# Performance work log

Measured on AMD Instinct MI355X. Metric: run time of the kernel, lower is better.

Reference implementation:

```python
import jax, jax.numpy as jnp
import numpy as np
import math

B, S, HID = 1, 2048, 1024
H = 16
D = HID // H          # head_dim = 64
M = 128               # RFF num_features
SIGMA = 1.0
ALPHA = 0.9
NORMALIZE = True


def setup_inputs() -> dict:
    key = jax.random.key(0)
    ks = jax.random.split(key, 12)
    s = 1.0 / math.sqrt(HID)  # nn.Linear default-ish init scale
    inp = {
        "hidden_states": jax.random.normal(ks[0], (B, S, HID), dtype=jnp.float32),
        "attention_mask": jnp.zeros((B, 1, 1, S), dtype=jnp.float32),  # 0 = attend
        "Wq": jax.random.uniform(ks[1], (HID, HID), minval=-s, maxval=s, dtype=jnp.float32),
        "bq": jnp.zeros((HID,), dtype=jnp.float32),
        "Wk": jax.random.uniform(ks[2], (HID, HID), minval=-s, maxval=s, dtype=jnp.float32),
        "bk": jnp.zeros((HID,), dtype=jnp.float32),
        "Wv": jax.random.uniform(ks[3], (HID, HID), minval=-s, maxval=s, dtype=jnp.float32),
        "bv": jnp.zeros((HID,), dtype=jnp.float32),
        "Wo": jax.random.uniform(ks[4], (HID, HID), minval=-s, maxval=s, dtype=jnp.float32),
        "bo": jnp.zeros((HID,), dtype=jnp.float32),
        # RFF kernel params per head: omega ~ N(0, 1/sigma^2), phase b ~ U[0, 2pi]
        "omega": jax.random.normal(ks[5], (H, D, M), dtype=jnp.float32) / SIGMA,
        "rff_b": jax.random.uniform(ks[6], (H, M), minval=0.0, maxval=2.0 * math.pi, dtype=jnp.float32),
    }
    return inp


def _heads(x):
    # (B, S, HID) -> (B, H, S, D)
    return x.reshape(B, S, H, D).transpose(0, 2, 1, 3)


def _phi(x, omega, rff_b):
    # x: (B, H, S, D) -> (B, H, S, M) random Fourier features
    proj = jnp.einsum("bhsd,hdm->bhsm", x, omega) + rff_b[None, :, None, :]
    phi = math.sqrt(2.0 / M) * jnp.cos(proj)
    if NORMALIZE:
        phi = phi / (jnp.linalg.norm(phi, axis=-1, keepdims=True) + 1e-6)
    return phi


def reference(hidden_states, attention_mask, Wq, bq, Wk, bk, Wv, bv, Wo, bo, omega, rff_b):
    q = _heads(hidden_states @ Wq.T + bq)   # (B,H,S,D)
    k = _heads(hidden_states @ Wk.T + bk)
    v = _heads(hidden_states @ Wv.T + bv)

    qn = q / (jnp.linalg.norm(q, axis=-1, keepdims=True) + 1e-6)
    kn = k / (jnp.linalg.norm(k, axis=-1, keepdims=True) + 1e-6)

    dot_scores = jnp.einsum("bhqd,bhkd->bhqk", q, k)             # standard QK^T
    kernel_scores = jnp.einsum("bhqm,bhkm->bhqk",
                               _phi(qn, omega, rff_b),
                               _phi(kn, omega, rff_b))            # phi(Q)phi(K)^T

    scores = (ALPHA * dot_scores + (1.0 - ALPHA) * kernel_scores) / math.sqrt(D)
    scores = scores + attention_mask * -10000.0
    weights = jax.nn.softmax(scores, axis=-1)                     # dropout: eval mode (identity)

    context = jnp.einsum("bhqk,bhkd->bhqd", weights, v)
    context = context.transpose(0, 2, 1, 3).reshape(B, S, HID)
    return context @ Wo.T + bo
```

## Files before the change

kernel.cpp:

```cpp
#include <hip/hip_runtime.h>
#include <math.h>

#define S_LEN 2048
#define HID   1024
#define NH    16
#define HD    64
#define NM    128
#define CAUG  192
#define KSPL  4

constexpr float ALPHA = 0.9f;

typedef __attribute__((ext_vector_type(8))) short bf16x8;
typedef __attribute__((ext_vector_type(4))) short bf16x4;
typedef __attribute__((ext_vector_type(4))) float f32x4;
typedef __attribute__((ext_vector_type(4))) int   int4v;

#define MFMA(a,b,c) __builtin_amdgcn_mfma_f32_16x16x32_bf16(a,b,c,0,0,0)

static __device__ inline short f2bf(float f) {
    unsigned u = __float_as_uint(f);
    u += 0x7fffu + ((u >> 16) & 1u);
    return (short)(u >> 16);
}
static __device__ inline float bf2f(short s) {
    return __uint_as_float(((unsigned)(unsigned short)s) << 16);
}

__global__ __launch_bounds__(256)
void conv_kernel(const float* __restrict__ hs,
                 const float* __restrict__ Wq, const float* __restrict__ Wk,
                 const float* __restrict__ Wv, const float* __restrict__ Wo,
                 const float* __restrict__ omega,
                 short* __restrict__ hsb, short* __restrict__ wqb, short* __restrict__ wkb,
                 short* __restrict__ wvb, short* __restrict__ wob, short* __restrict__ omtb)
{
    int i = blockIdx.x * 256 + threadIdx.x;
    if (i >= 1605632) return;
    if (i >= 1572864) {
        int j = (i - 1572864) * 4;
        int h = j >> 13, rem = j & 8191;
        int d = rem >> 7, m = rem & 127;
        float4 v = *(const float4*)(omega + j);
        short* dst = omtb + ((h * 128 + m) << 6) + d;
        dst[0]       = f2bf(v.x);
        dst[64]      = f2bf(v.y);
        dst[128]     = f2bf(v.z);
        dst[192]     = f2bf(v.w);
        return;
    }
    const float* src; short* dst; int off;
    if (i < 524288) { src = hs; dst = hsb; off = i; }
    else {
        int j = i - 524288;
        int r = j >> 18;
        off = j & 262143;
        src = (r == 0) ? Wq : (r == 1) ? Wk : (r == 2) ? Wv : Wo;
        dst = (r == 0) ? wqb : (r == 1) ? wkb : (r == 2) ? wvb : wob;
    }
    float4 v = ((const float4*)src)[off];
    bf16x4 o; o[0] = f2bf(v.x); o[1] = f2bf(v.y); o[2] = f2bf(v.z); o[3] = f2bf(v.w);
    ((bf16x4*)dst)[off] = o;
}

__global__ __launch_bounds__(256)
void gemm_mfma(const short* __restrict__ A,
               const short* __restrict__ W0, const float* __restrict__ b0, void* C0,
               const short* __restrict__ W1, const float* __restrict__ b1, void* C1,
               const short* __restrict__ W2, const float* __restrict__ b2, void* C2,
               int m0_, int m1_, int m2_, int Mrows)
{
    const short* W; const float* bias; void* C; int mode;
    if (blockIdx.z == 0)      { W = W0; bias = b0; C = C0; mode = m0_; }
    else if (blockIdx.z == 1) { W = W1; bias = b1; C = C1; mode = m1_; }
    else                      { W = W2; bias = b2; C = C2; mode = m2_; }

    __shared__ short As[64][40];
    __shared__ short Bs[128][40];

    const int tid = threadIdx.x;
    const int wave = tid >> 6, lane = tid & 63;
    const int l15 = lane & 15, l4 = lane >> 4;
    const int wm = wave >> 1, wn = wave & 1;
    const int m0 = blockIdx.y * 64, n0 = blockIdx.x * 128;

    const int srow = tid >> 2;
    const int scol = (tid & 3) * 16;

    f32x4 acc[2][4];
#pragma unroll
    for (int i = 0; i < 2; ++i)
#pragma unroll
        for (int j = 0; j < 4; ++j) acc[i][j] = (f32x4){0.f,0.f,0.f,0.f};

    int4v apre, bpre0, bpre1;
    apre  = *(const int4v*)((const char*)A + (size_t)(m0 + srow) * 2048 + scol);
    bpre0 = *(const int4v*)((const char*)W + (size_t)(n0 + srow) * 2048 + scol);
    bpre1 = *(const int4v*)((const char*)W + (size_t)(n0 + 64 + srow) * 2048 + scol);

    for (int ks = 0; ks < 32; ++ks) {
        __syncthreads();
        *(int4v*)((char*)&As[0][0] + srow * 80 + scol) = apre;
        *(int4v*)((char*)&Bs[0][0] + srow * 80 + scol) = bpre0;
        *(int4v*)((char*)&Bs[0][0] + (64 + srow) * 80 + scol) = bpre1;
        __syncthreads();
        if (ks + 1 < 32) {
            const int kb = (ks + 1) * 64;
            apre  = *(const int4v*)((const char*)A + (size_t)(m0 + srow) * 2048 + kb + scol);
            bpre0 = *(const int4v*)((const char*)W + (size_t)(n0 + srow) * 2048 + kb + scol);
            bpre1 = *(const int4v*)((const char*)W + (size_t)(n0 + 64 + srow) * 2048 + kb + scol);
        }
        bf16x8 af[2], bf[4];
#pragma unroll
        for (int mi = 0; mi < 2; ++mi)
            af[mi] = *(const bf16x8*)((const char*)&As[0][0] + (wm*32 + mi*16 + l15) * 80 + l4*16);
#pragma unroll
        for (int nj = 0; nj < 4; ++nj)
            bf[nj] = *(const bf16x8*)((const char*)&Bs[0][0] + (wn*64 + nj*16 + l15) * 80 + l4*16);
#pragma unroll
        for (int mi = 0; mi < 2; ++mi)
#pragma unroll
            for (int nj = 0; nj < 4; ++nj)
                acc[mi][nj] = MFMA(af[mi], bf[nj], acc[mi][nj]);
    }

#pragma unroll
    for (int nj = 0; nj < 4; ++nj) {
        const int nglob = n0 + wn*64 + nj*16 + l15;
        const float bn = bias[nglob];
#pragma unroll
        for (int mi = 0; mi < 2; ++mi) {
            const int mbase = m0 + wm*32 + mi*16 + l4*4;
            if (mode == 0) {
#pragma unroll
                for (int r = 0; r < 4; ++r)
                    ((short*)C)[(size_t)(mbase + r) * 1024 + nglob] = f2bf(acc[mi][nj][r] + bn);
            } else if (mode == 1) {
                bf16x4 pk;
#pragma unroll
                for (int r = 0; r < 4; ++r) pk[r] = f2bf(acc[mi][nj][r] + bn);
                *(bf16x4*)((short*)C + (size_t)nglob * Mrows + mbase) = pk;
            } else {
#pragma unroll
                for (int r = 0; r < 4; ++r)
                    ((float*)C)[(size_t)(mbase + r) * 1024 + nglob] = acc[mi][nj][r] + bn;
            }
        }
    }
}

__global__ __launch_bounds__(256)
void phi2_kernel(const short* __restrict__ qbuf, const short* __restrict__ kbuf,
                 const short* __restrict__ omtb, const float* __restrict__ rffb,
                 short* __restrict__ Qa, short* __restrict__ Ka)
{
    __shared__ short om[128][72];
    __shared__ float bsh[128];

    const int src = blockIdx.z, h = blockIdx.y;
    const int s0 = blockIdx.x * 64;
    const short* X = src ? kbuf : qbuf;
    short* Out     = src ? Ka : Qa;
    const float fq   = src ? 1.0f : (ALPHA * 0.125f);
    const float fphi = src ? 1.0f : ((1.0f - ALPHA) * 0.125f);

    const int tid = threadIdx.x, wave = tid >> 6, lane = tid & 63;
    const int l15 = lane & 15, l4 = lane >> 4;

    {
        const char* gsrc = (const char*)(omtb + ((size_t)h << 13));
#pragma unroll
        for (int it = 0; it < 4; ++it) {
            int f = tid * 16 + it * 4096;
            int row = f >> 7, colb = f & 127;
            *(int4v*)((char*)&om[0][0] + row * 144 + colb) = *(const int4v*)(gsrc + f);
        }
        if (tid < 128) bsh[tid] = rffb[h * 128 + tid];
    }
    __syncthreads();

    const int srow = s0 + wave * 16 + l15;

    bf16x8 xf[2];
#pragma unroll
    for (int cs = 0; cs < 2; ++cs)
        xf[cs] = *(const bf16x8*)(X + (size_t)srow * HID + h * HD + cs * 32 + l4 * 8);

    float ss = 0.f;
#pragma unroll
    for (int cs = 0; cs < 2; ++cs)
#pragma unroll
        for (int j = 0; j < 8; ++j) { float v = bf2f(xf[cs][j]); ss = fmaf(v, v, ss); }
    ss += __shfl_xor(ss, 16);
    ss += __shfl_xor(ss, 32);
    const float inv = 1.0f / (sqrtf(ss) + 1e-6f);

    bf16x8 qn[2];
#pragma unroll
    for (int cs = 0; cs < 2; ++cs) {
        bf16x8 o, w;
#pragma unroll
        for (int j = 0; j < 8; ++j) {
            float v = bf2f(xf[cs][j]);
            o[j] = f2bf(v * inv);
            w[j] = f2bf(v * fq);
        }
        qn[cs] = o;
        *(bf16x8*)(Out + ((size_t)h * S_LEN + srow) * CAUG + cs * 32 + l4 * 8) = w;
    }

    f32x4 pacc[8];
#pragma unroll
    for (int t = 0; t < 8; ++t) pacc[t] = (f32x4){0.f,0.f,0.f,0.f};
#pragma unroll
    for (int t = 0; t < 8; ++t)
#pragma unroll
        for (int cs = 0; cs < 2; ++cs) {
            bf16x8 bf = *(const bf16x8*)((const char*)&om[0][0] + (t*16 + l15) * 144 + cs*64 + l4*16);
            pacc[t] = MFMA(qn[cs], bf, pacc[t]);
        }

    float ph[8][4];
    float ps[4] = {0.f, 0.f, 0.f, 0.f};
#pragma unroll
    for (int t = 0; t < 8; ++t) {
        const float bv = bsh[t * 16 + l15];
#pragma unroll
        for (int r = 0; r < 4; ++r) {
            float p = pacc[t][r] + bv;
            float c = 0.125f * __cosf(p);
            ph[t][r] = c;
            ps[r] = fmaf(c, c, ps[r]);
        }
    }
#pragma unroll
    for (int r = 0; r < 4; ++r) {
        ps[r] += __shfl_xor(ps[r], 1);
        ps[r] += __shfl_xor(ps[r], 2);
        ps[r] += __shfl_xor(ps[r], 4);
        ps[r] += __shfl_xor(ps[r], 8);
    }
    float inv2[4];
#pragma unroll
    for (int r = 0; r < 4; ++r) inv2[r] = fphi / (sqrtf(ps[r]) + 1e-6f);

#pragma unroll
    for (int t = 0; t < 8; ++t)
#pragma unroll
        for (int r = 0; r < 4; ++r)
            Out[((size_t)h * S_LEN + s0 + wave * 16 + l4 * 4 + r) * CAUG + 64 + t * 16 + l15]
                = f2bf(ph[t][r] * inv2[r]);
}

__global__ __launch_bounds__(128, 4)
void flash_mfma(const short* __restrict__ Qa, const short* __restrict__ Ka,
                const short* __restrict__ vt, const float* __restrict__ mask,
                short* __restrict__ Opart, float* __restrict__ Lpart)
{
    __shared__ char smem[20480];

    const int tid = threadIdx.x;
    const int wave = tid >> 6, lane = tid & 63;
    const int l15 = lane & 15, l4 = lane >> 4;
    const int h = blockIdx.y, ksp = blockIdx.z;
    const int q0 = blockIdx.x * 64 + wave * 32;

    char* Kbuf = smem;
    char* Vbuf = smem + 12288;
    char* Pb   = smem + 16384 + wave * 2048;

    bf16x8 qf[2][6];
#pragma unroll
    for (int qj = 0; qj < 2; ++qj)
#pragma unroll
        for (int cs = 0; cs < 6; ++cs)
            qf[qj][cs] = *(const bf16x8*)(Qa + ((size_t)h * 2048 + q0 + qj*16 + l15) * CAUG + cs*32 + l4*8);

    f32x4 oacc[4][2];
#pragma unroll
    for (int di = 0; di < 4; ++di)
#pragma unroll
        for (int qj = 0; qj < 2; ++qj) oacc[di][qj] = (f32x4){0.f,0.f,0.f,0.f};
    float lsum[2] = {0.f, 0.f};

    int gK[6], wrK[6];
#pragma unroll
    for (int it = 0; it < 6; ++it) {
        int f = tid * 16 + it * 2048;
        int row = f / 384, col = f - row * 384;
        gK[it] = f;
        wrK[it] = row * 384 + (col ^ ((row & 7) << 4));
    }
    int gVrow[2], gVcol[2], wrV[2];
#pragma unroll
    for (int it = 0; it < 2; ++it) {
        int f = tid * 16 + it * 2048;
        int row = f >> 6, col = f & 63;
        gVrow[it] = row; gVcol[it] = col;
        wrV[it] = row * 64 + (col ^ ((row & 3) << 4));
    }

    const char* Kg = (const char*)(Ka + (size_t)h * 2048 * CAUG);
    const char* Vg = (const char*)(vt + (size_t)h * 64 * 2048);
    const int base = ksp * 16;
    const int swP = (l15 & 3) << 4;
    const int swK = (l15 & 7) << 4;

    for (int i = 0; i < 16; ++i) {
        const int kt = base + i;
        int4v kv[6], vv[2];
        const char* kb = Kg + (size_t)kt * 12288;
#pragma unroll
        for (int it = 0; it < 6; ++it)
            kv[it] = *(const int4v*)(kb + gK[it]);
#pragma unroll
        for (int it = 0; it < 2; ++it)
            vv[it] = *(const int4v*)(Vg + (size_t)gVrow[it] * 4096 + kt * 64 + gVcol[it]);
        __syncthreads();
#pragma unroll
        for (int it = 0; it < 6; ++it) *(int4v*)(Kbuf + wrK[it]) = kv[it];
#pragma unroll
        for (int it = 0; it < 2; ++it) *(int4v*)(Vbuf + wrV[it]) = vv[it];
        __syncthreads();

        f32x4 sacc[2][2];
#pragma unroll
        for (int fi = 0; fi < 2; ++fi)
#pragma unroll
            for (int qj = 0; qj < 2; ++qj) sacc[fi][qj] = (f32x4){0.f,0.f,0.f,0.f};
#pragma unroll
        for (int cs = 0; cs < 6; ++cs) {
            bf16x8 ka[2];
#pragma unroll
            for (int fi = 0; fi < 2; ++fi)
                ka[fi] = *(const bf16x8*)(Kbuf + (fi*16 + l15)*384 + ((cs*64 + l4*16) ^ swK));
#pragma unroll
            for (int fi = 0; fi < 2; ++fi)
#pragma unroll
                for (int qj = 0; qj < 2; ++qj)
                    sacc[fi][qj] = MFMA(ka[fi], qf[qj][cs], sacc[fi][qj]);
        }
#pragma unroll
        for (int fi = 0; fi < 2; ++fi) {
            float4 mk = *(const float4*)&mask[kt*32 + fi*16 + l4*4];
            float mv[4] = {mk.x * -10000.f, mk.y * -10000.f, mk.z * -10000.f, mk.w * -10000.f};
#pragma unroll
            for (int qj = 0; qj < 2; ++qj) {
                bf16x4 pk;
#pragma unroll
                for (int r = 0; r < 4; ++r) {
                    float p = __expf(sacc[fi][qj][r] + mv[r]);
                    lsum[qj] += p;
                    pk[r] = f2bf(p);
                }
                *(bf16x4*)(Pb + (qj*16 + l15)*64 + ((fi*32 + l4*8) ^ swP)) = pk;
            }
        }
        {
            bf16x8 pb[2];
#pragma unroll
            for (int qj = 0; qj < 2; ++qj)
                pb[qj] = *(const bf16x8*)(Pb + (qj*16 + l15)*64 + ((l4*16) ^ swP));
#pragma unroll
            for (int di = 0; di < 4; ++di) {
                const int vrow = di*16 + l15;
                bf16x8 va = *(const bf16x8*)(Vbuf + vrow*64 + ((l4*16) ^ ((vrow & 3) << 4)));
#pragma unroll
                for (int qj = 0; qj < 2; ++qj)
                    oacc[di][qj] = MFMA(va, pb[qj], oacc[di][qj]);
            }
        }
    }

#pragma unroll
    for (int qj = 0; qj < 2; ++qj) {
        lsum[qj] += __shfl_xor(lsum[qj], 16);
        lsum[qj] += __shfl_xor(lsum[qj], 32);
    }

    const size_t obase = (size_t)(ksp * NH + h) * 2048 + q0;
#pragma unroll
    for (int qj = 0; qj < 2; ++qj) {
        const size_t orow = obase + qj*16 + l15;
#pragma unroll
        for (int di = 0; di < 4; ++di) {
            bf16x4 ob;
#pragma unroll
            for (int r = 0; r < 4; ++r) ob[r] = f2bf(oacc[di][qj][r]);
            *(bf16x4*)(Opart + orow * 64 + di*16 + l4*4) = ob;
        }
        if (l4 == 0) Lpart[orow] = lsum[qj];
    }
}

__global__ __launch_bounds__(256)
void merge_kernel(const short* __restrict__ Opart, const float* __restrict__ Lpart,
                  short* __restrict__ ctxb)
{
    int tt = blockIdx.x * 256 + threadIdx.x;
    int e = tt * 4;
    int d = e & 63;
    int q = (e >> 6) & 2047;
    int h = e >> 17;
    float acc[4] = {0.f, 0.f, 0.f, 0.f};
    float L = 0.f;
#pragma unroll
    for (int s = 0; s < KSPL; ++s) {
        size_t idx = (size_t)(s * NH + h) * 2048 + q;
        bf16x4 a = *(const bf16x4*)(Opart + idx * 64 + d);
        L += Lpart[idx];
#pragma unroll
        for (int r = 0; r < 4; ++r) acc[r] += bf2f(a[r]);
    }
    float inv = 1.0f / L;
    bf16x4 o;
#pragma unroll
    for (int r = 0; r < 4; ++r) o[r] = f2bf(acc[r] * inv);
    *(bf16x4*)(ctxb + (size_t)q * 1024 + h * 64 + d) = o;
}

extern "C" void kernel_launch(void* const* d_in, const int* in_sizes, int n_in,
                              void* d_out, int out_size, void* d_ws, size_t ws_size,
                              hipStream_t stream)
{
    const float* hs    = (const float*)d_in[0];
    const float* mask  = (const float*)d_in[1];
    const float* Wq    = (const float*)d_in[2];
    const float* bq    = (const float*)d_in[3];
    const float* Wk    = (const float*)d_in[4];
    const float* bk    = (const float*)d_in[5];
    const float* Wv    = (const float*)d_in[6];
    const float* bv    = (const float*)d_in[7];
    const float* Wo    = (const float*)d_in[8];
    const float* bo    = (const float*)d_in[9];
    const float* omega = (const float*)d_in[10];
    const float* rffb  = (const float*)d_in[11];
    float* out = (float*)d_out;

    short* wsS  = (short*)d_ws;
    short* hsb  = wsS;
    short* wqb  = hsb + 2097152;
    short* wkb  = wqb + 1048576;
    short* wvb  = wkb + 1048576;
    short* wob  = wvb + 1048576;
    short* qb   = wob + 1048576;
    short* kb   = qb  + 2097152;
    short* vtb  = kb  + 2097152;
    short* ctxb = vtb + 2097152;
    short* QaB  = ctxb+ 2097152;
    short* KaB  = QaB + 6291456;
    short* omtb = KaB + 6291456;
    short* OpS  = omtb+ 131072;
    float* LpF  = (float*)(OpS + 8388608);

    conv_kernel<<<6272, 256, 0, stream>>>(hs, Wq, Wk, Wv, Wo, omega,
                                          hsb, wqb, wkb, wvb, wob, omtb);
    gemm_mfma<<<dim3(8, 32, 3), 256, 0, stream>>>(hsb, wqb, bq, qb, wkb, bk, kb, wvb, bv, vtb,
                                                  0, 0, 1, S_LEN);
    phi2_kernel<<<dim3(32, 16, 2), 256, 0, stream>>>(qb, kb, omtb, rffb, QaB, KaB);
    flash_mfma<<<dim3(32, 16, KSPL), 128, 0, stream>>>(QaB, KaB, vtb, mask, OpS, LpF);
    merge_kernel<<<2048, 256, 0, stream>>>(OpS, LpF, ctxb);
    gemm_mfma<<<dim3(8, 32, 1), 256, 0, stream>>>(ctxb, wob, bo, out, wob, bo, out, wob, bo, out,
                                                  2, 2, 2, S_LEN);
}
```

Measured before the change: 135.8 us.

## Switch flash attention kernel to 32x32x16 MFMA with in-register P via permlane swap

Rewrites the attention inner loop to use 32x32x16 bf16 MFMA tiles, one per wave covering 32 queries. The softmax probabilities are packed with v_cvt_pk_bf16_f32 and rearranged with v_permlane32_swap, so the P tile no longer goes through shared memory. K and V LDS layouts change to match: K is stored unswizzled and V uses a padded 80-byte row stride, and LDS use shrinks. This aims to cut LDS traffic and MFMA instruction count, at the cost of more registers (launch bounds lowered to 3 blocks per SM) and possible LDS bank conflicts from dropping the swizzle.

```diff
diff --git a/kernel.cpp b/kernel.cpp
--- a/kernel.cpp
+++ b/kernel.cpp
@@ -11,12 +11,14 @@
 
 constexpr float ALPHA = 0.9f;
 
-typedef __attribute__((ext_vector_type(8))) short bf16x8;
-typedef __attribute__((ext_vector_type(4))) short bf16x4;
-typedef __attribute__((ext_vector_type(4))) float f32x4;
-typedef __attribute__((ext_vector_type(4))) int   int4v;
-
-#define MFMA(a,b,c) __builtin_amdgcn_mfma_f32_16x16x32_bf16(a,b,c,0,0,0)
+typedef __attribute__((ext_vector_type(8)))  short bf16x8;
+typedef __attribute__((ext_vector_type(4)))  short bf16x4;
+typedef __attribute__((ext_vector_type(4)))  float f32x4;
+typedef __attribute__((ext_vector_type(16))) float f32x16;
+typedef __attribute__((ext_vector_type(4)))  int   int4v;
+
+#define MFMA(a,b,c)   __builtin_amdgcn_mfma_f32_16x16x32_bf16(a,b,c,0,0,0)
+#define MFMA32(a,b,c) __builtin_amdgcn_mfma_f32_32x32x16_bf16(a,b,c,0,0,0)
 
 static __device__ inline short f2bf(float f) {
     unsigned u = __float_as_uint(f);
@@ -25,6 +27,12 @@
 }
 static __device__ inline float bf2f(short s) {
     return __uint_as_float(((unsigned)(unsigned short)s) << 16);
+}
+static __device__ inline f32x16 zero16() {
+    f32x16 z;
+#pragma unroll
+    for (int j = 0; j < 16; ++j) z[j] = 0.f;
+    return z;
 }
 
 __global__ __launch_bounds__(256)
@@ -252,145 +260,122 @@
                 = f2bf(ph[t][r] * inv2[r]);
 }
 
-__global__ __launch_bounds__(128, 4)
+__global__ __launch_bounds__(128, 3)
 void flash_mfma(const short* __restrict__ Qa, const short* __restrict__ Ka,
                 const short* __restrict__ vt, const float* __restrict__ mask,
                 short* __restrict__ Opart, float* __restrict__ Lpart)
 {
-    __shared__ char smem[20480];
+    __shared__ char smem[17408];
+    char* Kbuf = smem;
+    char* Vbuf = smem + 12288;
 
     const int tid = threadIdx.x;
     const int wave = tid >> 6, lane = tid & 63;
-    const int l15 = lane & 15, l4 = lane >> 4;
-    const int h = blockIdx.y, ksp = blockIdx.z;
+    const int l31 = lane & 31, h = lane >> 5;
+    const int hd = blockIdx.y, ksp = blockIdx.z;
     const int q0 = blockIdx.x * 64 + wave * 32;
 
-    char* Kbuf = smem;
-    char* Vbuf = smem + 12288;
-    char* Pb   = smem + 16384 + wave * 2048;
-
-    bf16x8 qf[2][6];
-#pragma unroll
-    for (int qj = 0; qj < 2; ++qj)
-#pragma unroll
-        for (int cs = 0; cs < 6; ++cs)
-            qf[qj][cs] = *(const bf16x8*)(Qa + ((size_t)h * 2048 + q0 + qj*16 + l15) * CAUG + cs*32 + l4*8);
-
-    f32x4 oacc[4][2];
-#pragma unroll
-    for (int di = 0; di < 4; ++di)
-#pragma unroll
-        for (int qj = 0; qj < 2; ++qj) oacc[di][qj] = (f32x4){0.f,0.f,0.f,0.f};
-    float lsum[2] = {0.f, 0.f};
-
-    int gK[6], wrK[6];
+    bf16x8 qf[12];
+    {
+        const char* qrow = (const char*)Qa + ((size_t)hd * 2048 + q0 + l31) * 384 + h * 16;
+#pragma unroll
+        for (int cs = 0; cs < 12; ++cs)
+            qf[cs] = *(const bf16x8*)(qrow + cs * 32);
+    }
+
+    f32x16 oacc0 = zero16(), oacc1 = zero16();
+    float lsum = 0.f;
+
+    int gK[6];
 #pragma unroll
     for (int it = 0; it < 6; ++it) {
-        int f = tid * 16 + it * 2048;
-        int row = f / 384, col = f - row * 384;
-        gK[it] = f;
-        wrK[it] = row * 384 + (col ^ ((row & 7) << 4));
-    }
-    int gVrow[2], gVcol[2], wrV[2];
-#pragma unroll
-    for (int it = 0; it < 2; ++it) {
-        int f = tid * 16 + it * 2048;
-        int row = f >> 6, col = f & 63;
-        gVrow[it] = row; gVcol[it] = col;
-        wrV[it] = row * 64 + (col ^ ((row & 3) << 4));
-    }
-
-    const char* Kg = (const char*)(Ka + (size_t)h * 2048 * CAUG);
-    const char* Vg = (const char*)(vt + (size_t)h * 64 * 2048);
+        int L = (it * 128 + tid) * 16;
+        int cs = L >> 10, rem = L & 1023;
+        gK[it] = (rem >> 5) * 384 + cs * 32 + (rem & 16);
+    }
+    int gVrow[3], vcolA[3], wV[3];
+#pragma unroll
+    for (int it = 0; it < 3; ++it) {
+        int p = (it * 128 + tid) * 16;
+        int vr = p / 80, vc = p - vr * 80;
+        gVrow[it] = vr; vcolA[it] = vc; wV[it] = vr * 80 + vc;
+    }
+    const bool v2ok = (tid < 64);
+
+    const char* Kg = (const char*)Ka + (size_t)hd * 2048 * 384;
+    const char* Vg = (const char*)vt + (size_t)hd * 64 * 4096;
     const int base = ksp * 16;
-    const int swP = (l15 & 3) << 4;
-    const int swK = (l15 & 7) << 4;
 
     for (int i = 0; i < 16; ++i) {
         const int kt = base + i;
-        int4v kv[6], vv[2];
-        const char* kb = Kg + (size_t)kt * 12288;
+        int4v kv[6];
+        {
+            const char* kb = Kg + (size_t)kt * 12288;
+#pragma unroll
+            for (int it = 0; it < 6; ++it) kv[it] = *(const int4v*)(kb + gK[it]);
+        }
+        int4v vv0 = *(const int4v*)(Vg + (size_t)gVrow[0] * 4096 + kt * 64 + vcolA[0]);
+        int4v vv1 = *(const int4v*)(Vg + (size_t)gVrow[1] * 4096 + kt * 64 + vcolA[1]);
+        int4v vv2;
+        if (v2ok) vv2 = *(const int4v*)(Vg + (size_t)gVrow[2] * 4096 + kt * 64 + vcolA[2]);
+        __syncthreads();
 #pragma unroll
         for (int it = 0; it < 6; ++it)
-            kv[it] = *(const int4v*)(kb + gK[it]);
-#pragma unroll
-        for (int it = 0; it < 2; ++it)
-            vv[it] = *(const int4v*)(Vg + (size_t)gVrow[it] * 4096 + kt * 64 + gVcol[it]);
+            *(int4v*)(Kbuf + (it * 128 + tid) * 16) = kv[it];
+        *(int4v*)(Vbuf + wV[0]) = vv0;
+        *(int4v*)(Vbuf + wV[1]) = vv1;
+        if (v2ok) *(int4v*)(Vbuf + wV[2]) = vv2;
         __syncthreads();
-#pragma unroll
-        for (int it = 0; it < 6; ++it) *(int4v*)(Kbuf + wrK[it]) = kv[it];
-#pragma unroll
-        for (int it = 0; it < 2; ++it) *(int4v*)(Vbuf + wrV[it]) = vv[it];
-        __syncthreads();
-
-        f32x4 sacc[2][2];
-#pragma unroll
-        for (int fi = 0; fi < 2; ++fi)
-#pragma unroll
-            for (int qj = 0; qj < 2; ++qj) sacc[fi][qj] = (f32x4){0.f,0.f,0.f,0.f};
-#pragma unroll
-        for (int cs = 0; cs < 6; ++cs) {
-            bf16x8 ka[2];
-#pragma unroll
-            for (int fi = 0; fi < 2; ++fi)
-                ka[fi] = *(const bf16x8*)(Kbuf + (fi*16 + l15)*384 + ((cs*64 + l4*16) ^ swK));
-#pragma unroll
-            for (int fi = 0; fi < 2; ++fi)
-#pragma unroll
-                for (int qj = 0; qj < 2; ++qj)
-                    sacc[fi][qj] = MFMA(ka[fi], qf[qj][cs], sacc[fi][qj]);
-        }
-#pragma unroll
-        for (int fi = 0; fi < 2; ++fi) {
-            float4 mk = *(const float4*)&mask[kt*32 + fi*16 + l4*4];
-            float mv[4] = {mk.x * -10000.f, mk.y * -10000.f, mk.z * -10000.f, mk.w * -10000.f};
-#pragma unroll
-            for (int qj = 0; qj < 2; ++qj) {
-                bf16x4 pk;
-#pragma unroll
-                for (int r = 0; r < 4; ++r) {
-                    float p = __expf(sacc[fi][qj][r] + mv[r]);
-                    lsum[qj] += p;
-                    pk[r] = f2bf(p);
-                }
-                *(bf16x4*)(Pb + (qj*16 + l15)*64 + ((fi*32 + l4*8) ^ swP)) = pk;
-            }
-        }
-        {
-            bf16x8 pb[2];
-#pragma unroll
-            for (int qj = 0; qj < 2; ++qj)
-                pb[qj] = *(const bf16x8*)(Pb + (qj*16 + l15)*64 + ((l4*16) ^ swP));
-#pragma unroll
-            for (int di = 0; di < 4; ++di) {
-                const int vrow = di*16 + l15;
-                bf16x8 va = *(const bf16x8*)(Vbuf + vrow*64 + ((l4*16) ^ ((vrow & 3) << 4)));
-#pragma unroll
-                for (int qj = 0; qj < 2; ++qj)
-                    oacc[di][qj] = MFMA(va, pb[qj], oacc[di][qj]);
-            }
-        }
-    }
-
-#pragma unroll
-    for (int qj = 0; qj < 2; ++qj) {
-        lsum[qj] += __shfl_xor(lsum[qj], 16);
-        lsum[qj] += __shfl_xor(lsum[qj], 32);
-    }
-
-    const size_t obase = (size_t)(ksp * NH + h) * 2048 + q0;
-#pragma unroll
-    for (int qj = 0; qj < 2; ++qj) {
-        const size_t orow = obase + qj*16 + l15;
-#pragma unroll
-        for (int di = 0; di < 4; ++di) {
-            bf16x4 ob;
-#pragma unroll
-            for (int r = 0; r < 4; ++r) ob[r] = f2bf(oacc[di][qj][r]);
-            *(bf16x4*)(Opart + orow * 64 + di*16 + l4*4) = ob;
-        }
-        if (l4 == 0) Lpart[orow] = lsum[qj];
-    }
+
+        f32x16 sacc = zero16();
+#pragma unroll
+        for (int cs = 0; cs < 12; ++cs) {
+            bf16x8 ka = *(const bf16x8*)(Kbuf + cs * 1024 + l31 * 32 + h * 16);
+            sacc = MFMA32(ka, qf[cs], sacc);
+        }
+
+#pragma unroll
+        for (int t2 = 0; t2 < 2; ++t2) {
+            float4 mka = *(const float4*)&mask[kt * 32 + t2 * 16 + h * 4];
+            float4 mkb = *(const float4*)&mask[kt * 32 + t2 * 16 + 8 + h * 4];
+            float e0 = __expf(sacc[t2*8 + 0] + mka.x * -10000.f);
+            float e1 = __expf(sacc[t2*8 + 1] + mka.y * -10000.f);
+            float e2 = __expf(sacc[t2*8 + 2] + mka.z * -10000.f);
+            float e3 = __expf(sacc[t2*8 + 3] + mka.w * -10000.f);
+            float e4 = __expf(sacc[t2*8 + 4] + mkb.x * -10000.f);
+            float e5 = __expf(sacc[t2*8 + 5] + mkb.y * -10000.f);
+            float e6 = __expf(sacc[t2*8 + 6] + mkb.z * -10000.f);
+            float e7 = __expf(sacc[t2*8 + 7] + mkb.w * -10000.f);
+            lsum += ((e0 + e1) + (e2 + e3)) + ((e4 + e5) + (e6 + e7));
+            unsigned a0, a1, b0, b1;
+            asm("v_cvt_pk_bf16_f32 %0, %1, %2" : "=v"(a0) : "v"(e0), "v"(e1));
+            asm("v_cvt_pk_bf16_f32 %0, %1, %2" : "=v"(a1) : "v"(e2), "v"(e3));
+            asm("v_cvt_pk_bf16_f32 %0, %1, %2" : "=v"(b0) : "v"(e4), "v"(e5));
+            asm("v_cvt_pk_bf16_f32 %0, %1, %2" : "=v"(b1) : "v"(e6), "v"(e7));
+            asm volatile("v_permlane32_swap_b32 %0, %1" : "+v"(a0), "+v"(b0));
+            asm volatile("v_permlane32_swap_b32 %0, %1" : "+v"(a1), "+v"(b1));
+            union { int4v i; bf16x8 b; } pu;
+            pu.i[0] = (int)a0; pu.i[1] = (int)a1; pu.i[2] = (int)b0; pu.i[3] = (int)b1;
+            bf16x8 pb = pu.b;
+            bf16x8 va0 = *(const bf16x8*)(Vbuf + (l31)      * 80 + t2 * 32 + h * 16);
+            bf16x8 va1 = *(const bf16x8*)(Vbuf + (32 + l31) * 80 + t2 * 32 + h * 16);
+            oacc0 = MFMA32(va0, pb, oacc0);
+            oacc1 = MFMA32(va1, pb, oacc1);
+        }
+    }
+
+    lsum += __shfl_xor(lsum, 32);
+
+    const size_t orow = (size_t)(ksp * NH + hd) * 2048 + q0 + l31;
+#pragma unroll
+    for (int g = 0; g < 4; ++g) {
+        bf16x4 o0, o1;
+#pragma unroll
+        for (int r = 0; r < 4; ++r) { o0[r] = f2bf(oacc0[g*4 + r]); o1[r] = f2bf(oacc1[g*4 + r]); }
+        *(bf16x4*)(Opart + orow * 64 + g * 8 + h * 4)      = o0;
+        *(bf16x4*)(Opart + orow * 64 + 32 + g * 8 + h * 4) = o1;
+    }
+    if (lane < 32) Lpart[orow] = lsum;
 }
 
 __global__ __launch_bounds__(256)
```

Result: slower. 138.8 us (+2.2%).
